# Optimization experiments

Measured on AMD Instinct MI355X. Metric: run time of the kernel, lower is better.

Reference implementation:

```python
import jax, jax.numpy as jnp
import numpy as np

H = 768
NH = 12
HD = H // NH
FF = 3072
E = 4
EPS = 1e-12


def _make_expert_params(key):
    ks = jax.random.split(key, 8)
    s = 0.02
    return {
        'wq': jax.random.normal(ks[0], (H, H), jnp.float32) * s,
        'wk': jax.random.normal(ks[1], (H, H), jnp.float32) * s,
        'wv': jax.random.normal(ks[2], (H, H), jnp.float32) * s,
        'wo': jax.random.normal(ks[3], (H, H), jnp.float32) * s,
        'bq': jnp.zeros((H,), jnp.float32),
        'bk': jnp.zeros((H,), jnp.float32),
        'bv': jnp.zeros((H,), jnp.float32),
        'bo': jnp.zeros((H,), jnp.float32),
        'ln1_g': jnp.ones((H,), jnp.float32),
        'ln1_b': jnp.zeros((H,), jnp.float32),
        'w1': jax.random.normal(ks[4], (H, FF), jnp.float32) * s,
        'b1': jnp.zeros((FF,), jnp.float32),
        'w2': jax.random.normal(ks[5], (FF, H), jnp.float32) * s,
        'b2': jnp.zeros((H,), jnp.float32),
        'ln2_g': jnp.ones((H,), jnp.float32),
        'ln2_b': jnp.zeros((H,), jnp.float32),
    }


def setup_inputs() -> dict:
    key = jax.random.key(0)
    k1, k2, kp = jax.random.split(key, 3)
    hidden_states = jax.random.normal(k1, (64, 128, H), jnp.float32)
    attention_mask = jnp.zeros((64, 128), jnp.float32)  # additive mask, 0 = attend
    centers = jax.random.normal(k2, (E, H), jnp.float32)
    pkeys = jax.random.split(kp, E)
    ps = [_make_expert_params(k) for k in pkeys]
    # stack expert params along leading axis for vectorized gather-by-expert
    params = {k: jnp.stack([p[k] for p in ps], axis=0) for k in ps[0]}
    out = {'hidden_states': hidden_states, 'attention_mask': attention_mask, 'centers': centers}
    out.update(params)
    return out


def _layernorm(x, g, b):
    mu = x.mean(-1, keepdims=True)
    var = ((x - mu) ** 2).mean(-1, keepdims=True)
    return (x - mu) * jax.lax.rsqrt(var + EPS) * g + b


def _encoder(x, mask, p):
    # x: [B,S,H], mask: [B,S] additive; p: per-sample expert params (leading dim B)
    B, S, _ = x.shape
    q = jnp.einsum('bsh,bhd->bsd', x, p['wq']) + p['bq'][:, None, :]
    k = jnp.einsum('bsh,bhd->bsd', x, p['wk']) + p['bk'][:, None, :]
    v = jnp.einsum('bsh,bhd->bsd', x, p['wv']) + p['bv'][:, None, :]
    q = q.reshape(B, S, NH, HD)
    k = k.reshape(B, S, NH, HD)
    v = v.reshape(B, S, NH, HD)
    scores = jnp.einsum('bqnd,bknd->bnqk', q, k) / np.sqrt(HD).astype(np.float32)
    scores = scores + mask[:, None, None, :]
    attn = jax.nn.softmax(scores, axis=-1)
    ctx = jnp.einsum('bnqk,bknd->bqnd', attn, v).reshape(B, S, H)
    att_out = jnp.einsum('bsh,bhd->bsd', ctx, p['wo']) + p['bo'][:, None, :]
    att_out = _layernorm(att_out + x, p['ln1_g'][:, None, :], p['ln1_b'][:, None, :])
    ffn = jnp.einsum('bsh,bhf->bsf', att_out, p['w1']) + p['b1'][:, None, :]
    ffn = jax.nn.gelu(ffn)
    ffn = jnp.einsum('bsf,bfh->bsh', ffn, p['w2']) + p['b2'][:, None, :]
    out = _layernorm(att_out + ffn, p['ln2_g'][:, None, :], p['ln2_b'][:, None, :])
    return out


def reference(hidden_states, attention_mask, centers,
              wq, wk, wv, wo, bq, bk, bv, bo, ln1_g, ln1_b,
              w1, b1, w2, b2, ln2_g, ln2_b):
    # routing: mean over seq, cdist to centers, argmin -> per-sentence expert id
    h_pca = hidden_states.mean(axis=1)  # [B,H]
    d2 = (jnp.sum(h_pca ** 2, -1, keepdims=True)
          - 2.0 * h_pca @ centers.T
          + jnp.sum(centers ** 2, -1)[None, :])
    eid = jnp.argmin(d2, axis=1)  # [B]
    params = {'wq': wq, 'wk': wk, 'wv': wv, 'wo': wo, 'bq': bq, 'bk': bk,
              'bv': bv, 'bo': bo, 'ln1_g': ln1_g, 'ln1_b': ln1_b,
              'w1': w1, 'b1': b1, 'w2': w2, 'b2': b2,
              'ln2_g': ln2_g, 'ln2_b': ln2_b}
    # gather per-sample expert params (jit-friendly, honors hard routing)
    psel = {k: v[eid] for k, v in params.items()}
    return _encoder(hidden_states, attention_mask, psel)
```

## Files before the change

kernel.cpp:

```cpp
#include <hip/hip_runtime.h>
#include <hip/hip_bf16.h>
#include <math.h>

#define HDIM 768
#define NHEAD 12
#define HEADD 64
#define FFDIM 3072
#define NEXP 4
#define SEQ 128
#define NB 64
#define QKVN 2304

typedef __attribute__((ext_vector_type(8))) _Float16 f16x8;
typedef __attribute__((ext_vector_type(4))) _Float16 f16x4;
typedef __attribute__((ext_vector_type(4))) float f32x4;

#define WAITVM3 __builtin_amdgcn_s_waitcnt(0xF73)
#define WAITVM0 __builtin_amdgcn_s_waitcnt(0xF70)
#define WAITLGKM0 __builtin_amdgcn_s_waitcnt(0xC07F)

__device__ __forceinline__ float gelu_fast(float x) {
  float t = -1.5957691216057308f * x * __builtin_fmaf(0.044715f * x, x, 1.0f);
  return x * __builtin_amdgcn_rcpf(1.0f + __expf(t));
}

__device__ __forceinline__ void gld_lds16(const void* g, void* l) {
  __builtin_amdgcn_global_load_lds(
      (const __attribute__((address_space(1))) unsigned int*)g,
      (__attribute__((address_space(3))) unsigned int*)l, 16, 0, 0);
}

__global__ __launch_bounds__(256) void route_cvt_kernel(
    const float* __restrict__ hs, const float* __restrict__ centers,
    int* __restrict__ eid, _Float16* __restrict__ x16) {
  int b = blockIdx.x, t = threadIdx.x;
  __shared__ float hp[HDIM];
  __shared__ float dist[NEXP];
  const float* xb = hs + (size_t)b * SEQ * HDIM;
  _Float16* ob = x16 + (size_t)b * SEQ * HDIM;

  if (t < 192) {
    float p0 = 0.f, p1 = 0.f, p2 = 0.f, p3 = 0.f;
    for (int sq = 0; sq < SEQ; ++sq) {
      float4 v = ((const float4*)(xb + (size_t)sq * HDIM))[t];
      p0 += v.x; p1 += v.y; p2 += v.z; p3 += v.w;
      f16x4 h = {(_Float16)v.x, (_Float16)v.y, (_Float16)v.z, (_Float16)v.w};
      *(f16x4*)(ob + (size_t)sq * HDIM + t * 4) = h;
    }
    hp[t * 4 + 0] = p0 * (1.0f / SEQ);
    hp[t * 4 + 1] = p1 * (1.0f / SEQ);
    hp[t * 4 + 2] = p2 * (1.0f / SEQ);
    hp[t * 4 + 3] = p3 * (1.0f / SEQ);
  }
  if (t < NEXP) dist[t] = 0.f;
  __syncthreads();

  float pe[NEXP] = {0.f, 0.f, 0.f, 0.f};
  for (int h = t; h < HDIM; h += 256) {
    float v = hp[h];
#pragma unroll
    for (int e = 0; e < NEXP; ++e) {
      float d = v - centers[e * HDIM + h];
      pe[e] += d * d;
    }
  }
#pragma unroll
  for (int e = 0; e < NEXP; ++e) atomicAdd(&dist[e], pe[e]);
  __syncthreads();
  if (t == 0) {
    int best = 0; float bv = dist[0];
    for (int e = 1; e < NEXP; ++e) if (dist[e] < bv) { bv = dist[e]; best = e; }
    eid[b] = best;
  }
}

__device__ __forceinline__ void tr_tile(const float* __restrict__ ip,
                                        _Float16* __restrict__ op,
                                        int K, int N, int nb, int kb,
                                        float (*tile)[33], int t) {
  int tx = t & 31, ty = t >> 5;
  for (int i = ty; i < 32; i += 8)
    tile[i][tx] = ip[(size_t)(kb + i) * N + nb + tx];
  __syncthreads();
  for (int i = ty; i < 32; i += 8)
    op[(size_t)(nb + i) * K + kb + tx] = (_Float16)tile[tx][i];
}

__global__ __launch_bounds__(256) void prep_weights(
    const float* __restrict__ wq, const float* __restrict__ wk,
    const float* __restrict__ wv, const float* __restrict__ wo,
    const float* __restrict__ w1, const float* __restrict__ w2,
    const float* __restrict__ bq, const float* __restrict__ bk,
    const float* __restrict__ bv,
    _Float16* __restrict__ Wqkvt, _Float16* __restrict__ Wot,
    _Float16* __restrict__ W1t, _Float16* __restrict__ W2t,
    float* __restrict__ bqkv, const int* __restrict__ eid,
    int* __restrict__ order, int* __restrict__ ord_eid) {
  __shared__ float tile[32][33];
  int x = blockIdx.x, e = blockIdx.y, t = threadIdx.x;

  if (x < 1728) {
    int which = x / 576, local = x % 576;
    const float* src = (which == 0) ? wq : (which == 1) ? wk : wv;
    tr_tile(src + (size_t)e * HDIM * HDIM,
            Wqkvt + (size_t)which * HDIM * HDIM + (size_t)e * QKVN * HDIM,
            HDIM, HDIM, (local % 24) * 32, (local / 24) * 32, tile, t);
  } else if (x < 2304) {
    int local = x - 1728;
    tr_tile(wo + (size_t)e * HDIM * HDIM, Wot + (size_t)e * HDIM * HDIM,
            HDIM, HDIM, (local % 24) * 32, (local / 24) * 32, tile, t);
  } else if (x < 4608) {
    int local = x - 2304;
    tr_tile(w1 + (size_t)e * HDIM * FFDIM, W1t + (size_t)e * FFDIM * HDIM,
            HDIM, FFDIM, (local % 96) * 32, (local / 96) * 32, tile, t);
  } else if (x < 6912) {
    int local = x - 4608;
    tr_tile(w2 + (size_t)e * FFDIM * HDIM, W2t + (size_t)e * HDIM * FFDIM,
            FFDIM, HDIM, (local % 24) * 32, (local / 24) * 32, tile, t);
  } else if (x < 6948) {
    if (e == 0) {
      int i = (x - 6912) * 256 + t;
      if (i < NEXP * QKVN) {
        int ee = i / QKVN, n = i % QKVN;
        float v = (n < HDIM) ? bq[ee * HDIM + n]
                : (n < 2 * HDIM) ? bk[ee * HDIM + n - HDIM]
                                 : bv[ee * HDIM + n - 2 * HDIM];
        bqkv[i] = v;
      }
    }
  } else {
    if (e == 0 && t == 0) {
      int n = 0;
      for (int ee = 0; ee < NEXP; ++ee)
        for (int b = 0; b < NB; ++b)
          if (eid[b] == ee) { order[n] = b; ord_eid[n] = ee; n++; }
    }
  }
}

template <int OUT_F16, int GELU, int KDIM, int SPLITK>
__global__ __launch_bounds__(512, 2) void gemm_mfma8(
    const _Float16* __restrict__ A, const _Float16* __restrict__ Wt,
    const float* __restrict__ Ball, const int* __restrict__ order,
    const int* __restrict__ ord_eid, void* __restrict__ Cv, int N) {
  constexpr int K = KDIM;
  constexpr int Kp = KDIM / SPLITK;
  constexpr int NT = Kp / 64;
  extern __shared__ __align__(16) char dynlds[];
  _Float16* lds = (_Float16*)dynlds;

  int GX = N >> 8;
  int nwg = GX * NB * SPLITK;
  int L = blockIdx.x;
  int r = (L & 7) * (nwg >> 3) + (L >> 3);
  int z = r & 63;
  int rest = r >> 6;
  int kz = rest % SPLITK;
  int c = rest / SPLITK;
  int b = order[z];
  int e = ord_eid[z];
  int col0 = c * 256;
  int kbeg = kz * Kp;

  int t = threadIdx.x;
  int lane = t & 63, w = t >> 6;
  int quad = lane >> 4, l16 = lane & 15;
  int wr64 = (w >> 2) * 64;
  int wc64 = (w & 3) * 64;

  int csw = ((t & 3) ^ ((t >> 2) & 3) ^ ((t >> 4) & 3)) * 8;
  int r0 = t >> 2;

  const _Float16* srcA = A + (size_t)b * SEQ * K + kbeg + (size_t)r0 * K + csw;
  const _Float16* srcB0 = Wt + (size_t)e * N * K + (size_t)(col0 + r0) * K + kbeg + csw;
  const _Float16* srcB1 = srcB0 + (size_t)128 * K;

  auto issueH = [&](int Tn, int h) {
    _Float16* dst = lds + (size_t)(Tn & 1) * 24576;
    int goff = Tn * 64 + h * 32;
    gld_lds16(srcA + goff, dst + h * 4096 + t * 8);
    gld_lds16(srcB0 + goff, dst + 8192 + h * 8192 + t * 8);
    gld_lds16(srcB1 + goff, dst + 8192 + h * 8192 + 4096 + t * 8);
  };

  f32x4 acc[4][4];
#pragma unroll
  for (int i = 0; i < 4; ++i)
#pragma unroll
    for (int j = 0; j < 4; ++j) acc[i][j] = (f32x4){0.f, 0.f, 0.f, 0.f};

  int sl = (l16 & 3) ^ ((l16 >> 2) & 3);
  int ck8 = (quad ^ sl) * 8;

  issueH(0, 0);
  issueH(0, 1);
  WAITVM3;
  __builtin_amdgcn_s_barrier();

#pragma unroll 2
  for (int T = 0; T < NT; ++T) {
    int bi = T & 1;
    const _Float16* Ab = lds + (size_t)bi * 24576;
    const _Float16* Bb = Ab + 8192;

    {
      f16x8 af[4], bf[4];
#pragma unroll
      for (int i = 0; i < 4; ++i)
        af[i] = *(const f16x8*)&Ab[(wr64 + i * 16 + l16) * 32 + ck8];
#pragma unroll
      for (int j = 0; j < 4; ++j)
        bf[j] = *(const f16x8*)&Bb[(wc64 + j * 16 + l16) * 32 + ck8];
      if (T + 1 < NT) issueH(T + 1, 0);
      __builtin_amdgcn_s_barrier();
      WAITLGKM0;
      __builtin_amdgcn_s_setprio(1);
#pragma unroll
      for (int i = 0; i < 4; ++i)
#pragma unroll
        for (int j = 0; j < 4; ++j)
          acc[i][j] = __builtin_amdgcn_mfma_f32_16x16x32_f16(af[i], bf[j], acc[i][j], 0, 0, 0);
      __builtin_amdgcn_s_setprio(0);
      if (T + 1 < NT) WAITVM3;
      else            WAITVM0;
      __builtin_amdgcn_s_barrier();
    }

    {
      const _Float16* Ab1 = Ab + 4096;
      const _Float16* Bb1 = Bb + 8192;
      f16x8 af[4], bf[4];
#pragma unroll
      for (int i = 0; i < 4; ++i)
        af[i] = *(const f16x8*)&Ab1[(wr64 + i * 16 + l16) * 32 + ck8];
#pragma unroll
      for (int j = 0; j < 4; ++j)
        bf[j] = *(const f16x8*)&Bb1[(wc64 + j * 16 + l16) * 32 + ck8];
      if (T + 1 < NT) issueH(T + 1, 1);
      __builtin_amdgcn_s_barrier();
      WAITLGKM0;
      __builtin_amdgcn_s_setprio(1);
#pragma unroll
      for (int i = 0; i < 4; ++i)
#pragma unroll
        for (int j = 0; j < 4; ++j)
          acc[i][j] = __builtin_amdgcn_mfma_f32_16x16x32_f16(af[i], bf[j], acc[i][j], 0, 0, 0);
      __builtin_amdgcn_s_setprio(0);
      if (T + 1 < NT) {
        WAITVM3;
        __builtin_amdgcn_s_barrier();
      }
    }
  }

  const float* bias = Ball + (size_t)e * N;

  if (OUT_F16) {
    _Float16* Ch = (_Float16*)Cv + (size_t)b * SEQ * N;
#pragma unroll
    for (int i = 0; i < 4; ++i)
#pragma unroll
      for (int j = 0; j < 4; ++j) {
        int col = col0 + wc64 + j * 16 + l16;
        float bv = bias[col];
#pragma unroll
        for (int r2 = 0; r2 < 4; ++r2) {
          int row = wr64 + i * 16 + quad * 4 + r2;
          float v = acc[i][j][r2] + bv;
          if (GELU) v = gelu_fast(v);
          Ch[(size_t)row * N + col] = (_Float16)v;
        }
      }
  } else {
    float* Cf = (float*)Cv + (size_t)kz * NB * SEQ * N + (size_t)b * SEQ * N;
    float bscale = (kz == 0) ? 1.f : 0.f;
#pragma unroll
    for (int i = 0; i < 4; ++i)
#pragma unroll
      for (int j = 0; j < 4; ++j) {
        int col = col0 + wc64 + j * 16 + l16;
        float bv = bias[col] * bscale;
#pragma unroll
        for (int r2 = 0; r2 < 4; ++r2) {
          int row = wr64 + i * 16 + quad * 4 + r2;
          Cf[(size_t)row * N + col] = acc[i][j][r2] + bv;
        }
      }
  }
}

__global__ __launch_bounds__(256) void attn_mfma(
    const _Float16* __restrict__ QKV, const float* __restrict__ mask,
    _Float16* __restrict__ Ctx) {
  int h = blockIdx.x, b = blockIdx.y;
  int t = threadIdx.x;
  int w = t >> 6, lane = t & 63, quad = lane >> 4, l16 = lane & 15;

  __shared__ __align__(16) char smem[54784];
  _Float16* Qs = (_Float16*)smem;
  _Float16* Ks = (_Float16*)(smem + 18432);
  _Float16* Ps = (_Float16*)smem;
  _Float16* Vt = (_Float16*)(smem + 36864);
  float* mrow = (float*)(smem + 54272);

  const _Float16* Qb = QKV + (size_t)b * SEQ * QKVN + h * HEADD;
  const _Float16* Kb = Qb + HDIM;
  const _Float16* Vb = Qb + 2 * HDIM;

#pragma unroll
  for (int it = 0; it < 4; ++it) {
    int chunk = t + it * 256;
    int row = chunk >> 3, c = chunk & 7;
    *(f16x8*)&Qs[row * 72 + c * 8] = *(const f16x8*)(Qb + (size_t)row * QKVN + c * 8);
    *(f16x8*)&Ks[row * 72 + c * 8] = *(const f16x8*)(Kb + (size_t)row * QKVN + c * 8);
  }
  {
    int vc = t & 7, vjp0 = t >> 3;
#pragma unroll
    for (int it = 0; it < 2; ++it) {
      int jp = vjp0 + it * 32;
      f16x8 v0 = *(const f16x8*)(Vb + (size_t)(2 * jp) * QKVN + vc * 8);
      f16x8 v1 = *(const f16x8*)(Vb + (size_t)(2 * jp + 1) * QKVN + vc * 8);
#pragma unroll
      for (int i = 0; i < 8; ++i) {
        int d = vc * 8 + i;
        unsigned ua = __builtin_bit_cast(unsigned short, (_Float16)v0[i]);
        unsigned ub = __builtin_bit_cast(unsigned short, (_Float16)v1[i]);
        ((unsigned*)Vt)[d * 68 + jp] = ua | (ub << 16);
      }
    }
  }
  if (t < SEQ) mrow[t] = mask[(size_t)b * SEQ + t];
  __syncthreads();

  int m0 = w * 32;
  f32x4 accs[2][8];
#pragma unroll
  for (int i = 0; i < 2; ++i)
#pragma unroll
    for (int j = 0; j < 8; ++j) accs[i][j] = (f32x4){0.f, 0.f, 0.f, 0.f};

#pragma unroll
  for (int ks = 0; ks < 2; ++ks) {
    int k0 = ks * 32 + quad * 8;
    f16x8 af[2], bf[8];
#pragma unroll
    for (int i = 0; i < 2; ++i)
      af[i] = *(const f16x8*)&Qs[(m0 + i * 16 + l16) * 72 + k0];
#pragma unroll
    for (int j = 0; j < 8; ++j)
      bf[j] = *(const f16x8*)&Ks[(j * 16 + l16) * 72 + k0];
#pragma unroll
    for (int i = 0; i < 2; ++i)
#pragma unroll
      for (int j = 0; j < 8; ++j)
        accs[i][j] = __builtin_amdgcn_mfma_f32_16x16x32_f16(af[i], bf[j], accs[i][j], 0, 0, 0);
  }
  __syncthreads();

  float mv[8];
#pragma unroll
  for (int j = 0; j < 8; ++j) mv[j] = mrow[j * 16 + l16];

  float linv[2][4];
#pragma unroll
  for (int i = 0; i < 2; ++i) {
#pragma unroll
    for (int j = 0; j < 8; ++j)
#pragma unroll
      for (int r = 0; r < 4; ++r)
        accs[i][j][r] = accs[i][j][r] * 0.125f + mv[j];
#pragma unroll
    for (int r = 0; r < 4; ++r) {
      float m = accs[i][0][r];
#pragma unroll
      for (int j = 1; j < 8; ++j) m = fmaxf(m, accs[i][j][r]);
      m = fmaxf(m, __shfl_xor(m, 1));
      m = fmaxf(m, __shfl_xor(m, 2));
      m = fmaxf(m, __shfl_xor(m, 4));
      m = fmaxf(m, __shfl_xor(m, 8));
      float sum = 0.f;
#pragma unroll
      for (int j = 0; j < 8; ++j) {
        float p = __expf(accs[i][j][r] - m);
        accs[i][j][r] = p;
        sum += p;
      }
      sum += __shfl_xor(sum, 1);
      sum += __shfl_xor(sum, 2);
      sum += __shfl_xor(sum, 4);
      sum += __shfl_xor(sum, 8);
      linv[i][r] = 1.f / sum;
    }
    int rowb = m0 + i * 16 + quad * 4;
#pragma unroll
    for (int j = 0; j < 8; ++j)
#pragma unroll
      for (int r = 0; r < 4; ++r)
        Ps[(rowb + r) * 136 + j * 16 + l16] = (_Float16)accs[i][j][r];
  }
  __syncthreads();

  f32x4 acco[2][4];
#pragma unroll
  for (int i = 0; i < 2; ++i)
#pragma unroll
    for (int j = 0; j < 4; ++j) acco[i][j] = (f32x4){0.f, 0.f, 0.f, 0.f};

#pragma unroll
  for (int ks = 0; ks < 4; ++ks) {
    int k0 = ks * 32 + quad * 8;
    f16x8 pa[2], vf[4];
#pragma unroll
    for (int i = 0; i < 2; ++i)
      pa[i] = *(const f16x8*)&Ps[(m0 + i * 16 + l16) * 136 + k0];
#pragma unroll
    for (int j = 0; j < 4; ++j)
      vf[j] = *(const f16x8*)&Vt[(j * 16 + l16) * 136 + k0];
#pragma unroll
    for (int i = 0; i < 2; ++i)
#pragma unroll
      for (int j = 0; j < 4; ++j)
        acco[i][j] = __builtin_amdgcn_mfma_f32_16x16x32_f16(pa[i], vf[j], acco[i][j], 0, 0, 0);
  }

  _Float16* Cb = Ctx + (size_t)b * SEQ * HDIM + h * HEADD;
#pragma unroll
  for (int i = 0; i < 2; ++i)
#pragma unroll
    for (int j = 0; j < 4; ++j)
#pragma unroll
      for (int r = 0; r < 4; ++r) {
        int row = m0 + i * 16 + quad * 4 + r;
        int d = j * 16 + l16;
        Cb[(size_t)row * HDIM + d] = (_Float16)(acco[i][j][r] * linv[i][r]);
      }
}

template <int NP>
__global__ __launch_bounds__(256) void resid_ln_kernel(
    const float* __restrict__ X, const float* __restrict__ P0,
    const float* __restrict__ P1,
    const float* __restrict__ Gall, const float* __restrict__ Ball,
    const int* __restrict__ eid, float* __restrict__ Out,
    _Float16* __restrict__ Out16) {
  int row = blockIdx.x, b = blockIdx.y, t = threadIdx.x;
  int e = eid[b];
  size_t off = ((size_t)b * SEQ + row) * HDIM;
  const float* x = X + off;
  const float* p0 = P0 + off;
  const float* p1 = (NP > 1) ? P1 + off : nullptr;
  float* o = Out + off;
  const float* g = Gall + (size_t)e * HDIM;
  const float* bb = Ball + (size_t)e * HDIM;

  __shared__ float buf[HDIM];
  __shared__ float red[256];

  float s = 0.f;
  for (int h = t; h < HDIM; h += 256) {
    float v = x[h] + p0[h];
    if (NP > 1) v += p1[h];
    buf[h] = v;
    s += v;
  }
  red[t] = s;
  __syncthreads();
  for (int off2 = 128; off2 > 0; off2 >>= 1) {
    if (t < off2) red[t] += red[t + off2];
    __syncthreads();
  }
  float mean = red[0] * (1.0f / HDIM);
  __syncthreads();

  float s2 = 0.f;
  for (int h = t; h < HDIM; h += 256) {
    float d = buf[h] - mean;
    s2 += d * d;
  }
  red[t] = s2;
  __syncthreads();
  for (int off2 = 128; off2 > 0; off2 >>= 1) {
    if (t < off2) red[t] += red[t + off2];
    __syncthreads();
  }
  float var = red[0] * (1.0f / HDIM);
  float rs = rsqrtf(var + 1e-12f);

  for (int h = t; h < HDIM; h += 256) {
    float v = (buf[h] - mean) * rs * g[h] + bb[h];
    o[h] = v;
    if (Out16) Out16[off + h] = (_Float16)v;
  }
}

extern "C" void kernel_launch(void* const* d_in, const int* in_sizes, int n_in,
                              void* d_out, int out_size, void* d_ws, size_t ws_size,
                              hipStream_t stream) {
  const float* hs   = (const float*)d_in[0];
  const float* mask = (const float*)d_in[1];
  const float* cen  = (const float*)d_in[2];
  const float* wq = (const float*)d_in[3];
  const float* wk = (const float*)d_in[4];
  const float* wv = (const float*)d_in[5];
  const float* wo = (const float*)d_in[6];
  const float* bq = (const float*)d_in[7];
  const float* bk = (const float*)d_in[8];
  const float* bv = (const float*)d_in[9];
  const float* bo = (const float*)d_in[10];
  const float* ln1g = (const float*)d_in[11];
  const float* ln1b = (const float*)d_in[12];
  const float* w1 = (const float*)d_in[13];
  const float* b1 = (const float*)d_in[14];
  const float* w2 = (const float*)d_in[15];
  const float* b2 = (const float*)d_in[16];
  const float* ln2g = (const float*)d_in[17];
  const float* ln2b = (const float*)d_in[18];
  float* out = (float*)d_out;

  const size_t sh = (size_t)SEQ * HDIM;
  const int DYNLDS = 98304;

  static bool attr_done = false;
  if (!attr_done) {
    attr_done = true;
    auto* k1 = gemm_mfma8<1, 0, HDIM, 1>;
    auto* k2 = gemm_mfma8<0, 0, HDIM, 2>;
    auto* k3 = gemm_mfma8<1, 1, HDIM, 1>;
    auto* k4 = gemm_mfma8<0, 0, FFDIM, 2>;
    (void)hipFuncSetAttribute((const void*)k1, hipFuncAttributeMaxDynamicSharedMemorySize, DYNLDS);
    (void)hipFuncSetAttribute((const void*)k2, hipFuncAttributeMaxDynamicSharedMemorySize, DYNLDS);
    (void)hipFuncSetAttribute((const void*)k3, hipFuncAttributeMaxDynamicSharedMemorySize, DYNLDS);
    (void)hipFuncSetAttribute((const void*)k4, hipFuncAttributeMaxDynamicSharedMemorySize, DYNLDS);
  }

  char* p = (char*)d_ws;
  int* eid = (int*)p;                 p += 256;
  int* order = (int*)p;               p += 256;
  int* ord_eid = (int*)p;             p += 256;
  float* bqkv = (float*)p;            p += (size_t)NEXP * QKVN * 4;
  _Float16* Wqkvt = (_Float16*)p;     p += (size_t)NEXP * QKVN * HDIM * 2;
  _Float16* Wot = (_Float16*)p;       p += (size_t)NEXP * HDIM * HDIM * 2;
  _Float16* W1t = (_Float16*)p;       p += (size_t)NEXP * FFDIM * HDIM * 2;
  _Float16* W2t = (_Float16*)p;       p += (size_t)NEXP * HDIM * FFDIM * 2;
  _Float16* x16 = (_Float16*)p;       p += (size_t)NB * sh * 2;

  char* region = p;                   p += (size_t)NB * SEQ * QKVN * 2;
  _Float16* ctx16 = (_Float16*)p;     p += (size_t)NB * sh * 2;
  float* aof = (float*)p;             p += (size_t)NB * sh * 4;
  _Float16* ao16 = (_Float16*)p;      p += (size_t)NB * sh * 2;
  char* ffreg = p;                    p += (size_t)NB * SEQ * FFDIM * 2;

  float* woparts = (float*)ffreg;
  float* w2parts = (float*)region;
  _Float16* ff16 = (_Float16*)ffreg;

  route_cvt_kernel<<<NB, 256, 0, stream>>>(hs, cen, eid, x16);
  prep_weights<<<dim3(6949, NEXP), 256, 0, stream>>>(
      wq, wk, wv, wo, w1, w2, bq, bk, bv,
      Wqkvt, Wot, W1t, W2t, bqkv, eid, order, ord_eid);
  gemm_mfma8<1, 0, HDIM, 1><<<dim3((QKVN / 256) * NB), 512, DYNLDS, stream>>>(
      x16, Wqkvt, bqkv, order, ord_eid, region, QKVN);
  attn_mfma<<<dim3(NHEAD, NB), 256, 0, stream>>>(
      (const _Float16*)region, mask, ctx16);
  gemm_mfma8<0, 0, HDIM, 2><<<dim3((HDIM / 256) * NB * 2), 512, DYNLDS, stream>>>(
      ctx16, Wot, bo, order, ord_eid, woparts, HDIM);
  resid_ln_kernel<2><<<dim3(SEQ, NB), 256, 0, stream>>>(
      hs, woparts, woparts + (size_t)NB * sh, ln1g, ln1b, eid, aof, ao16);
  gemm_mfma8<1, 1, HDIM, 1><<<dim3((FFDIM / 256) * NB), 512, DYNLDS, stream>>>(
      ao16, W1t, b1, order, ord_eid, ff16, FFDIM);
  gemm_mfma8<0, 0, FFDIM, 2><<<dim3((HDIM / 256) * NB * 2), 512, DYNLDS, stream>>>(
      ff16, W2t, b2, order, ord_eid, w2parts, HDIM);
  resid_ln_kernel<2><<<dim3(SEQ, NB), 256, 0, stream>>>(
      aof, w2parts, w2parts + (size_t)NB * sh, ln2g, ln2b, eid, out,
      (_Float16*)nullptr);
}
```

Measured before the change: 488.8 us.

## Retile grouped GEMM to 128x192 tiles with 64-wide K stages

Changes the GEMM tile from 128x256 to 128x192 columns: each wave now covers 64x48 of the output, with a 4x3 accumulator array. The LDS stage is restructured to hold full 64-wide K rows with a new XOR swizzle, and loads are split into two phases. The two waits and barriers per stage are replaced by one full wait and barrier at the end of each stage. The goals are more workgroups (column counts now divide by 192), lower register and LDS use so occupancy hint 4 can apply, and less LDS per block. The cost is lower MFMA reuse per loaded byte and a coarser sync point that can expose global-load latency.

Measured after the change: 449.9 us. 8.0% less time.

```diff
diff --git a/kernel.cpp b/kernel.cpp
--- a/kernel.cpp
+++ b/kernel.cpp
@@ -15,7 +15,6 @@
 typedef __attribute__((ext_vector_type(4))) _Float16 f16x4;
 typedef __attribute__((ext_vector_type(4))) float f32x4;
 
-#define WAITVM3 __builtin_amdgcn_s_waitcnt(0xF73)
 #define WAITVM0 __builtin_amdgcn_s_waitcnt(0xF70)
 #define WAITLGKM0 __builtin_amdgcn_s_waitcnt(0xC07F)
 
@@ -139,7 +138,7 @@
 }
 
 template <int OUT_F16, int GELU, int KDIM, int SPLITK>
-__global__ __launch_bounds__(512, 2) void gemm_mfma8(
+__global__ __launch_bounds__(512, 4) void gemm_mfma8(
     const _Float16* __restrict__ A, const _Float16* __restrict__ Wt,
     const float* __restrict__ Ball, const int* __restrict__ order,
     const int* __restrict__ ord_eid, void* __restrict__ Cv, int N) {
@@ -149,7 +148,7 @@
   extern __shared__ __align__(16) char dynlds[];
   _Float16* lds = (_Float16*)dynlds;
 
-  int GX = N >> 8;
+  int GX = N / 192;
   int nwg = GX * NB * SPLITK;
   int L = blockIdx.x;
   int r = (L & 7) * (nwg >> 3) + (L >> 3);
@@ -159,97 +158,95 @@
   int c = rest / SPLITK;
   int b = order[z];
   int e = ord_eid[z];
-  int col0 = c * 256;
+  int col0 = c * 192;
   int kbeg = kz * Kp;
 
   int t = threadIdx.x;
   int lane = t & 63, w = t >> 6;
   int quad = lane >> 4, l16 = lane & 15;
   int wr64 = (w >> 2) * 64;
-  int wc64 = (w & 3) * 64;
-
-  int csw = ((t & 3) ^ ((t >> 2) & 3) ^ ((t >> 4) & 3)) * 8;
-  int r0 = t >> 2;
-
-  const _Float16* srcA = A + (size_t)b * SEQ * K + kbeg + (size_t)r0 * K + csw;
-  const _Float16* srcB0 = Wt + (size_t)e * N * K + (size_t)(col0 + r0) * K + kbeg + csw;
-  const _Float16* srcB1 = srcB0 + (size_t)128 * K;
-
-  auto issueH = [&](int Tn, int h) {
-    _Float16* dst = lds + (size_t)(Tn & 1) * 24576;
-    int goff = Tn * 64 + h * 32;
-    gld_lds16(srcA + goff, dst + h * 4096 + t * 8);
-    gld_lds16(srcB0 + goff, dst + 8192 + h * 8192 + t * 8);
-    gld_lds16(srcB1 + goff, dst + 8192 + h * 8192 + 4096 + t * 8);
+  int wc48 = (w & 3) * 48;
+
+  int srow = t >> 3;
+  int scol = ((t & 7) * 8) ^ ((t & 32) >> 1);
+
+  const _Float16* srcA = A + (size_t)b * SEQ * K + kbeg + (size_t)srow * K + scol;
+  const _Float16* srcB = Wt + (size_t)e * N * K + (size_t)(col0 + srow) * K + kbeg + scol;
+
+  auto issueP0 = [&](int Tn) {
+    _Float16* dst = lds + (size_t)(Tn & 1) * 20480;
+    int goff = Tn * 64;
+    gld_lds16(srcA + goff, dst + t * 8);
+    gld_lds16(srcA + (size_t)64 * K + goff, dst + 4096 + t * 8);
+    gld_lds16(srcB + goff, dst + 8192 + t * 8);
   };
-
-  f32x4 acc[4][4];
+  auto issueP1 = [&](int Tn) {
+    _Float16* dst = lds + (size_t)(Tn & 1) * 20480;
+    int goff = Tn * 64;
+    gld_lds16(srcB + (size_t)64 * K + goff, dst + 12288 + t * 8);
+    gld_lds16(srcB + (size_t)128 * K + goff, dst + 16384 + t * 8);
+  };
+
+  f32x4 acc[4][3];
 #pragma unroll
   for (int i = 0; i < 4; ++i)
 #pragma unroll
-    for (int j = 0; j < 4; ++j) acc[i][j] = (f32x4){0.f, 0.f, 0.f, 0.f};
-
-  int sl = (l16 & 3) ^ ((l16 >> 2) & 3);
-  int ck8 = (quad ^ sl) * 8;
-
-  issueH(0, 0);
-  issueH(0, 1);
-  WAITVM3;
+    for (int j = 0; j < 3; ++j) acc[i][j] = (f32x4){0.f, 0.f, 0.f, 0.f};
+
+  int ck = (quad * 8) ^ ((l16 & 4) << 2);
+
+  issueP0(0);
+  issueP1(0);
+  WAITVM0;
   __builtin_amdgcn_s_barrier();
 
-#pragma unroll 2
   for (int T = 0; T < NT; ++T) {
-    int bi = T & 1;
-    const _Float16* Ab = lds + (size_t)bi * 24576;
+    const _Float16* Ab = lds + (size_t)(T & 1) * 20480;
     const _Float16* Bb = Ab + 8192;
 
     {
-      f16x8 af[4], bf[4];
+      f16x8 af[4], bf[3];
 #pragma unroll
       for (int i = 0; i < 4; ++i)
-        af[i] = *(const f16x8*)&Ab[(wr64 + i * 16 + l16) * 32 + ck8];
-#pragma unroll
-      for (int j = 0; j < 4; ++j)
-        bf[j] = *(const f16x8*)&Bb[(wc64 + j * 16 + l16) * 32 + ck8];
-      if (T + 1 < NT) issueH(T + 1, 0);
+        af[i] = *(const f16x8*)&Ab[(wr64 + i * 16 + l16) * 64 + ck];
+#pragma unroll
+      for (int j = 0; j < 3; ++j)
+        bf[j] = *(const f16x8*)&Bb[(wc48 + j * 16 + l16) * 64 + ck];
+      if (T + 1 < NT) issueP0(T + 1);
       __builtin_amdgcn_s_barrier();
       WAITLGKM0;
       __builtin_amdgcn_s_setprio(1);
 #pragma unroll
       for (int i = 0; i < 4; ++i)
 #pragma unroll
-        for (int j = 0; j < 4; ++j)
+        for (int j = 0; j < 3; ++j)
           acc[i][j] = __builtin_amdgcn_mfma_f32_16x16x32_f16(af[i], bf[j], acc[i][j], 0, 0, 0);
       __builtin_amdgcn_s_setprio(0);
-      if (T + 1 < NT) WAITVM3;
-      else            WAITVM0;
-      __builtin_amdgcn_s_barrier();
     }
 
     {
-      const _Float16* Ab1 = Ab + 4096;
-      const _Float16* Bb1 = Bb + 8192;
-      f16x8 af[4], bf[4];
+      f16x8 af[4], bf[3];
 #pragma unroll
       for (int i = 0; i < 4; ++i)
-        af[i] = *(const f16x8*)&Ab1[(wr64 + i * 16 + l16) * 32 + ck8];
-#pragma unroll
-      for (int j = 0; j < 4; ++j)
-        bf[j] = *(const f16x8*)&Bb1[(wc64 + j * 16 + l16) * 32 + ck8];
-      if (T + 1 < NT) issueH(T + 1, 1);
+        af[i] = *(const f16x8*)&Ab[(wr64 + i * 16 + l16) * 64 + 32 + ck];
+#pragma unroll
+      for (int j = 0; j < 3; ++j)
+        bf[j] = *(const f16x8*)&Bb[(wc48 + j * 16 + l16) * 64 + 32 + ck];
+      if (T + 1 < NT) issueP1(T + 1);
       __builtin_amdgcn_s_barrier();
       WAITLGKM0;
       __builtin_amdgcn_s_setprio(1);
 #pragma unroll
       for (int i = 0; i < 4; ++i)
 #pragma unroll
-        for (int j = 0; j < 4; ++j)
+        for (int j = 0; j < 3; ++j)
           acc[i][j] = __builtin_amdgcn_mfma_f32_16x16x32_f16(af[i], bf[j], acc[i][j], 0, 0, 0);
       __builtin_amdgcn_s_setprio(0);
-      if (T + 1 < NT) {
-        WAITVM3;
-        __builtin_amdgcn_s_barrier();
-      }
+    }
+
+    if (T + 1 < NT) {
+      WAITVM0;
+      __builtin_amdgcn_s_barrier();
     }
   }
 
@@ -260,8 +257,8 @@
 #pragma unroll
     for (int i = 0; i < 4; ++i)
 #pragma unroll
-      for (int j = 0; j < 4; ++j) {
-        int col = col0 + wc64 + j * 16 + l16;
+      for (int j = 0; j < 3; ++j) {
+        int col = col0 + wc48 + j * 16 + l16;
         float bv = bias[col];
 #pragma unroll
         for (int r2 = 0; r2 < 4; ++r2) {
@@ -277,8 +274,8 @@
 #pragma unroll
     for (int i = 0; i < 4; ++i)
 #pragma unroll
-      for (int j = 0; j < 4; ++j) {
-        int col = col0 + wc64 + j * 16 + l16;
+      for (int j = 0; j < 3; ++j) {
+        int col = col0 + wc48 + j * 16 + l16;
         float bv = bias[col] * bscale;
 #pragma unroll
         for (int r2 = 0; r2 < 4; ++r2) {
@@ -519,7 +516,7 @@
   float* out = (float*)d_out;
 
   const size_t sh = (size_t)SEQ * HDIM;
-  const int DYNLDS = 98304;
+  const int DYNLDS = 81920;
 
   static bool attr_done = false;
   if (!attr_done) {
@@ -559,17 +556,17 @@
   prep_weights<<<dim3(6949, NEXP), 256, 0, stream>>>(
       wq, wk, wv, wo, w1, w2, bq, bk, bv,
       Wqkvt, Wot, W1t, W2t, bqkv, eid, order, ord_eid);
-  gemm_mfma8<1, 0, HDIM, 1><<<dim3((QKVN / 256) * NB), 512, DYNLDS, stream>>>(
+  gemm_mfma8<1, 0, HDIM, 1><<<dim3((QKVN / 192) * NB), 512, DYNLDS, stream>>>(
       x16, Wqkvt, bqkv, order, ord_eid, region, QKVN);
   attn_mfma<<<dim3(NHEAD, NB), 256, 0, stream>>>(
       (const _Float16*)region, mask, ctx16);
-  gemm_mfma8<0, 0, HDIM, 2><<<dim3((HDIM / 256) * NB * 2), 512, DYNLDS, stream>>>(
+  gemm_mfma8<0, 0, HDIM, 2><<<dim3((HDIM / 192) * NB * 2), 512, DYNLDS, stream>>>(
       ctx16, Wot, bo, order, ord_eid, woparts, HDIM);
   resid_ln_kernel<2><<<dim3(SEQ, NB), 256, 0, stream>>>(
       hs, woparts, woparts + (size_t)NB * sh, ln1g, ln1b, eid, aof, ao16);
-  gemm_mfma8<1, 1, HDIM, 1><<<dim3((FFDIM / 256) * NB), 512, DYNLDS, stream>>>(
+  gemm_mfma8<1, 1, HDIM, 1><<<dim3((FFDIM / 192) * NB), 512, DYNLDS, stream>>>(
       ao16, W1t, b1, order, ord_eid, ff16, FFDIM);
-  gemm_mfma8<0, 0, FFDIM, 2><<<dim3((HDIM / 256) * NB * 2), 512, DYNLDS, stream>>>(
+  gemm_mfma8<0, 0, FFDIM, 2><<<dim3((HDIM / 192) * NB * 2), 512, DYNLDS, stream>>>(
       ff16, W2t, b2, order, ord_eid, w2parts, HDIM);
   resid_ln_kernel<2><<<dim3(SEQ, NB), 256, 0, stream>>>(
       aof, w2parts, w2parts + (size_t)NB * sh, ln2g, ln2b, eid, out,
```
